# Kernel optimization log

Measured on AMD Instinct MI355X. Metric: run time of the kernel, lower is better.

## Reference

```python
import jax, jax.numpy as jnp
import numpy as np

NH = 16
D = 1024
DKH = D // NH  # 64


def _split_heads(x, nh):
    B, L, d = x.shape
    return x.reshape(B, L, nh, d // nh).transpose(0, 2, 1, 3)  # [B,Nh,L,dh]


def setup_inputs() -> dict:
    key = jax.random.key(0)
    ks = jax.random.split(key, 10)
    B, L, d = 2, 2048, D
    s = 1.0 / np.sqrt(d)
    inp = {
        "q": jax.random.normal(ks[0], (B, L, d), jnp.float32),
        "k": jax.random.normal(ks[1], (B, L, d), jnp.float32),
        "q_mask": jnp.ones((B, L), jnp.float32),
        "k_mask": jnp.ones((B, L), jnp.float32),
        "pos_logits": jax.random.normal(ks[2], (B, L, L), jnp.float32),
        # Linear params (torch convention: y = x @ W.T + b)
        "Wq": jax.random.normal(ks[3], (d, d), jnp.float32) * s,
        "bq": jnp.zeros((d,), jnp.float32),
        "Wk": jax.random.normal(ks[4], (d, d), jnp.float32) * s,
        "bk": jnp.zeros((d,), jnp.float32),
        "Wv": jax.random.normal(ks[5], (d, d), jnp.float32) * s,
        "bv": jnp.zeros((d,), jnp.float32),
        "Wo": jax.random.normal(ks[6], (d, d), jnp.float32) * s,
        "bo": jnp.zeros((d,), jnp.float32),
    }
    return inp


def reference(q, k, q_mask, k_mask, pos_logits, Wq, bq, Wk, bk, Wv, bv, Wo, bo):
    # Projections (note: v is computed from the *projected* k, as in the source)
    qp = (q @ Wq.T + bq) * (DKH ** -0.5)   # [B,Lq,dk]
    kp = k @ Wk.T + bk                     # [B,Lk,dk]
    vp = kp @ Wv.T + bv                    # [B,Lk,dv]

    qh = _split_heads(qp, NH)              # [B,Nh,Lq,dkh]
    kh = _split_heads(kp, NH)              # [B,Nh,Lk,dkh]
    vh = _split_heads(vp, NH)              # [B,Nh,Lk,dvh]

    # Additive attention mask: -inf where q_mask[i]*k_mask[j] == 0
    mask_prod = q_mask[:, :, None] * k_mask[:, None, :]          # [B,Lq,Lk]
    attn_mask = jnp.where(mask_prod == 0, jnp.float32(-jnp.inf), jnp.float32(0.0))[:, None]  # [B,1,Lq,Lk]

    con_logits = jnp.einsum("bhid,bhjd->bhij", qh, kh)           # [B,Nh,Lq,Lk]
    logits = attn_mask + con_logits + pos_logits[:, None]
    weights = jax.nn.softmax(logits, axis=-1)
    attn = jnp.einsum("bhij,bhjd->bhid", weights, vh)            # [B,Nh,Lq,dvh]

    B, Nh, Lq, dvh = attn.shape
    attn = attn.transpose(0, 2, 1, 3).reshape(B, Lq, Nh * dvh)   # combine heads
    out = attn @ Wo.T + bo                                       # output projection
    # dropout is identity in eval mode
    return out
```

## Files before the change

### kernel.cpp

```cpp
#include <hip/hip_runtime.h>
#include <math.h>

#define BB 2
#define LL 2048
#define DMODEL 1024
#define NHEAD 16
#define MTOK 4096
#define KVB 32
#define NT (LL / KVB)

typedef unsigned short u16;
typedef __attribute__((ext_vector_type(8))) short short8;
typedef __attribute__((ext_vector_type(4))) float f32x4;

__device__ __host__ inline u16 f2bf(float f) {
    unsigned u = __builtin_bit_cast(unsigned, f);
    return (u16)((u + 0x7FFFu + ((u >> 16) & 1u)) >> 16);
}
__device__ inline float bf2f(u16 h) {
    unsigned u = ((unsigned)h) << 16;
    return __builtin_bit_cast(float, u);
}

__device__ inline void split_one(const float* __restrict__ x, u16* __restrict__ hi,
                                 u16* __restrict__ lo, int n4)
{
    for (int i = blockIdx.x * blockDim.x + threadIdx.x; i < n4;
         i += gridDim.x * blockDim.x) {
        float4 v = ((const float4*)x)[i];
        ushort4 h, l;
        h.x = f2bf(v.x); l.x = f2bf(v.x - bf2f(h.x));
        h.y = f2bf(v.y); l.y = f2bf(v.y - bf2f(h.y));
        h.z = f2bf(v.z); l.z = f2bf(v.z - bf2f(h.z));
        h.w = f2bf(v.w); l.w = f2bf(v.w - bf2f(h.w));
        ((ushort4*)hi)[i] = h;
        ((ushort4*)lo)[i] = l;
    }
}

__global__ __launch_bounds__(256)
void split_planes2(const float* __restrict__ x0, u16* __restrict__ h0, u16* __restrict__ l0,
                   const float* __restrict__ x1, u16* __restrict__ h1, u16* __restrict__ l1,
                   int n4)
{
    if (blockIdx.y == 0) split_one(x0, h0, l0, n4);
    else                 split_one(x1, h1, l1, n4);
}

__global__ __launch_bounds__(256)
void split_planes4(const float* __restrict__ x0, u16* __restrict__ h0, u16* __restrict__ l0,
                   const float* __restrict__ x1, u16* __restrict__ h1, u16* __restrict__ l1,
                   const float* __restrict__ x2, u16* __restrict__ h2, u16* __restrict__ l2,
                   const float* __restrict__ x3, u16* __restrict__ h3, u16* __restrict__ l3,
                   int n4)
{
    switch (blockIdx.y & 3) {
        case 0: split_one(x0, h0, l0, n4); break;
        case 1: split_one(x1, h1, l1, n4); break;
        case 2: split_one(x2, h2, l2, n4); break;
        default: split_one(x3, h3, l3, n4); break;
    }
}

#define GBM 128
#define GBN 64
#define GBK 32

__global__ __launch_bounds__(256)
void gemm_mfma_split(const u16* __restrict__ Ahi, const u16* __restrict__ Alo,
                     const u16* __restrict__ Bhi, const u16* __restrict__ Blo,
                     const float* __restrict__ bias, float scale, int K, int N,
                     float* __restrict__ Yf, u16* __restrict__ Yhi,
                     u16* __restrict__ Ylo, int mode)
{
    __shared__ u16 lds[2][12288];

    const int tid = threadIdx.x;
    const int lid = tid & 63;
    const int w   = tid >> 6;
    const int wm  = w >> 1, wn = w & 1;
    const int m0  = blockIdx.y * GBM;
    const int n0  = blockIdx.x * GBN;

    f32x4 acc[4][2];
    #pragma unroll
    for (int ms = 0; ms < 4; ++ms)
        #pragma unroll
        for (int ns = 0; ns < 2; ++ns)
            acc[ms][ns] = (f32x4){0.f, 0.f, 0.f, 0.f};

    auto stage = [&](int buf, int t) {
        const int k0 = t * GBK;
        #pragma unroll
        for (int j = 0; j < 6; ++j) {
            const int q = w * 6 + j;
            const u16* plane; int ldsoff, c, R0;
            if (q < 8)       { plane = Ahi; ldsoff = 0;     c = q;      R0 = m0; }
            else if (q < 16) { plane = Alo; ldsoff = 4096;  c = q - 8;  R0 = m0; }
            else if (q < 20) { plane = Bhi; ldsoff = 8192;  c = q - 16; R0 = n0; }
            else             { plane = Blo; ldsoff = 10240; c = q - 20; R0 = n0; }
            const int r  = c * 16 + (lid >> 2);
            const int ci = lid & 3;
            const int kl = ci ^ ((r >> 1) & 3);
            const u16* g = plane + (size_t)(R0 + r) * K + k0 + kl * 8;
            __builtin_amdgcn_global_load_lds(
                (const __attribute__((address_space(1))) void*)g,
                (__attribute__((address_space(3))) void*)(&lds[buf][ldsoff + c * 512]),
                16, 0, 0);
        }
    };

    auto compute = [&](int buf) {
        const u16* L = lds[buf];
        short8 ah[4], al[4], bh[2], bl[2];
        #pragma unroll
        for (int ms = 0; ms < 4; ++ms) {
            const int r   = wm * 64 + ms * 16 + (lid & 15);
            const int off = r * 32 + (((lid >> 4) ^ ((r >> 1) & 3)) * 8);
            ah[ms] = *(const short8*)&L[off];
            al[ms] = *(const short8*)&L[4096 + off];
        }
        #pragma unroll
        for (int ns = 0; ns < 2; ++ns) {
            const int r   = wn * 32 + ns * 16 + (lid & 15);
            const int off = r * 32 + (((lid >> 4) ^ ((r >> 1) & 3)) * 8);
            bh[ns] = *(const short8*)&L[8192 + off];
            bl[ns] = *(const short8*)&L[10240 + off];
        }
        #pragma unroll
        for (int ms = 0; ms < 4; ++ms)
            #pragma unroll
            for (int ns = 0; ns < 2; ++ns) {
                acc[ms][ns] = __builtin_amdgcn_mfma_f32_16x16x32_bf16(al[ms], bh[ns], acc[ms][ns], 0, 0, 0);
                acc[ms][ns] = __builtin_amdgcn_mfma_f32_16x16x32_bf16(ah[ms], bl[ns], acc[ms][ns], 0, 0, 0);
                acc[ms][ns] = __builtin_amdgcn_mfma_f32_16x16x32_bf16(ah[ms], bh[ns], acc[ms][ns], 0, 0, 0);
            }
    };

    const int nt = K / GBK;
    stage(0, 0);
    __syncthreads();
    for (int t = 0; t < nt; ++t) {
        const int buf = t & 1;
        if (t + 1 < nt) stage(buf ^ 1, t + 1);
        compute(buf);
        __syncthreads();
    }

    const int orow = (lid >> 4) * 4;
    #pragma unroll
    for (int ms = 0; ms < 4; ++ms)
        #pragma unroll
        for (int ns = 0; ns < 2; ++ns) {
            const int col = n0 + wn * 32 + ns * 16 + (lid & 15);
            const float bcol = bias[col];
            if (mode == 2) {
                const int r0 = m0 + wm * 64 + ms * 16 + orow;
                unsigned ph[2] = {0, 0}, pl[2] = {0, 0};
                #pragma unroll
                for (int i = 0; i < 4; ++i) {
                    const float y = (acc[ms][ns][i] + bcol) * scale;
                    const u16 hh = f2bf(y);
                    const u16 ll = f2bf(y - bf2f(hh));
                    ph[i >> 1] |= ((unsigned)hh) << ((i & 1) * 16);
                    pl[i >> 1] |= ((unsigned)ll) << ((i & 1) * 16);
                }
                const size_t idx = (size_t)col * MTOK + r0;
                *(uint2*)(Yhi + idx) = make_uint2(ph[0], ph[1]);
                *(uint2*)(Ylo + idx) = make_uint2(pl[0], pl[1]);
            } else {
                #pragma unroll
                for (int i = 0; i < 4; ++i) {
                    const int row = m0 + wm * 64 + ms * 16 + orow + i;
                    const float y = (acc[ms][ns][i] + bcol) * scale;
                    if (mode == 0) {
                        Yf[(size_t)row * N + col] = y;
                    } else {
                        const size_t idx = (size_t)row * N + col;
                        const u16 hh = f2bf(y);
                        Yhi[idx] = hh;
                        Ylo[idx] = f2bf(y - bf2f(hh));
                    }
                }
            }
        }
}

__global__ __launch_bounds__(256, 4)
void attn_mfma3(const u16* __restrict__ qph, const u16* __restrict__ qpl,
                const u16* __restrict__ kph, const u16* __restrict__ kpl,
                const u16* __restrict__ vth, const u16* __restrict__ vtl,
                const float* __restrict__ qmask, const float* __restrict__ kmask,
                const float* __restrict__ pos,
                u16* __restrict__ ach, u16* __restrict__ acl)
{
    __shared__ float pp[4][512];
    __shared__ u16  kvb[2][4][2048];

    const int tid = threadIdx.x;
    const int lid = tid & 63;
    const int w   = tid >> 6;
    const int q16 = lid & 15;
    const int hi4 = lid >> 4;
    const int qt = blockIdx.x, h = blockIdx.y, b = blockIdx.z;
    const int qw = qt * 64 + w * 16;

    short8 qh[2], ql[2];
    #pragma unroll
    for (int ks = 0; ks < 2; ++ks) {
        const size_t off = (size_t)(b * LL + qw + q16) * DMODEL
                         + h * 64 + ks * 32 + hi4 * 8;
        qh[ks] = *(const short8*)(qph + off);
        ql[ks] = *(const short8*)(qpl + off);
    }

    auto stage = [&](int buf, int t) {
        const int k0 = t * KVB;
        u16* dst = &kvb[buf][w][0];
        #pragma unroll
        for (int c = 0; c < 4; ++c) {
            const u16* src;
            if (w < 2) {
                const int r  = c * 8 + (lid >> 3);
                const int sl = (lid & 7) ^ (r & 7);
                src = (w == 0 ? kph : kpl) +
                      (size_t)(b * LL + k0 + r) * DMODEL + h * 64 + sl * 8;
            } else {
                const int r  = c * 16 + (lid >> 2);
                const int sl = (lid & 3) ^ ((r >> 1) & 3);
                src = (w == 2 ? vth : vtl) +
                      (size_t)(h * 64 + r) * MTOK + b * LL + k0 + sl * 8;
            }
            __builtin_amdgcn_global_load_lds(
                (const __attribute__((address_space(1))) void*)src,
                (__attribute__((address_space(3))) void*)(dst + c * 512), 16, 0, 0);
        }
    };

    float m_run = -INFINITY, l_run = 0.f;
    const float qml = qmask[b * LL + qw + q16];

    f32x4 o_acc[4];
    #pragma unroll
    for (int nfd = 0; nfd < 4; ++nfd)
        o_acc[nfd] = (f32x4){0.f, 0.f, 0.f, 0.f};

    stage(0, 0);
    __syncthreads();

    for (int t = 0; t < NT; ++t) {
        const int buf = t & 1;
        const int k0  = t * KVB;

        float4 kmv[2], posr[2];
        #pragma unroll
        for (int nf = 0; nf < 2; ++nf) {
            kmv[nf]  = *(const float4*)(kmask + b * LL + k0 + nf * 16 + hi4 * 4);
            posr[nf] = *(const float4*)(pos +
                ((size_t)(b * LL + qw + q16)) * LL + k0 + nf * 16 + hi4 * 4);
        }

        if (t + 1 < NT) stage(buf ^ 1, t + 1);

        f32x4 s_acc[2];
        s_acc[0] = (f32x4){0.f, 0.f, 0.f, 0.f};
        s_acc[1] = (f32x4){0.f, 0.f, 0.f, 0.f};

        #pragma unroll
        for (int ks = 0; ks < 2; ++ks)
            #pragma unroll
            for (int nf = 0; nf < 2; ++nf) {
                const int r  = nf * 16 + q16;
                const int sl = (ks * 4 + hi4) ^ (r & 7);
                short8 kbh = *(const short8*)(&kvb[buf][0][r * 64 + sl * 8]);
                short8 kbl = *(const short8*)(&kvb[buf][1][r * 64 + sl * 8]);
                s_acc[nf] = __builtin_amdgcn_mfma_f32_16x16x32_bf16(kbl, qh[ks], s_acc[nf], 0, 0, 0);
                s_acc[nf] = __builtin_amdgcn_mfma_f32_16x16x32_bf16(kbh, ql[ks], s_acc[nf], 0, 0, 0);
                s_acc[nf] = __builtin_amdgcn_mfma_f32_16x16x32_bf16(kbh, qh[ks], s_acc[nf], 0, 0, 0);
            }

        {
            float v[2][4];
            #pragma unroll
            for (int nf = 0; nf < 2; ++nf) {
                const float* km = (const float*)&kmv[nf];
                const float* pr = (const float*)&posr[nf];
                #pragma unroll
                for (int i = 0; i < 4; ++i)
                    v[nf][i] = (qml * km[i] == 0.f)
                               ? -INFINITY : s_acc[nf][i] + pr[i];
            }
            float rm = fmaxf(fmaxf(fmaxf(v[0][0], v[0][1]), fmaxf(v[0][2], v[0][3])),
                             fmaxf(fmaxf(v[1][0], v[1][1]), fmaxf(v[1][2], v[1][3])));
            rm = fmaxf(rm, __shfl_xor(rm, 16));
            rm = fmaxf(rm, __shfl_xor(rm, 32));
            const float mn = fmaxf(m_run, rm);
            const float c  = __expf(m_run - mn);
            float ls = 0.f;
            float p[2][4];
            #pragma unroll
            for (int nf = 0; nf < 2; ++nf)
                #pragma unroll
                for (int i = 0; i < 4; ++i) {
                    p[nf][i] = __expf(v[nf][i] - mn);
                    ls += p[nf][i];
                }
            ls += __shfl_xor(ls, 16);
            ls += __shfl_xor(ls, 32);
            l_run = l_run * c + ls;
            m_run = mn;
            #pragma unroll
            for (int nfd = 0; nfd < 4; ++nfd)
                o_acc[nfd] *= c;
            const int r = q16;
            #pragma unroll
            for (int nf = 0; nf < 2; ++nf) {
                const int sl = (nf * 4 + hi4) ^ (r & 7);
                *(f32x4*)&pp[w][r * 32 + sl * 4] =
                    (f32x4){p[nf][0], p[nf][1], p[nf][2], p[nf][3]};
            }
        }

        short8 pah, pal;
        {
            const int r  = q16;
            const int s0 = (hi4 * 2)     ^ (r & 7);
            const int s1 = (hi4 * 2 + 1) ^ (r & 7);
            f32x4 pa = *(const f32x4*)&pp[w][r * 32 + s0 * 4];
            f32x4 pb = *(const f32x4*)&pp[w][r * 32 + s1 * 4];
            float f[8] = {pa[0], pa[1], pa[2], pa[3], pb[0], pb[1], pb[2], pb[3]};
            #pragma unroll
            for (int jj = 0; jj < 8; ++jj) {
                const unsigned u = __builtin_bit_cast(unsigned, f[jj]);
                pah[jj] = (short)(u >> 16);
                const float lof = f[jj] - __builtin_bit_cast(float, u & 0xFFFF0000u);
                pal[jj] = (short)(__builtin_bit_cast(unsigned, lof) >> 16);
            }
        }
        #pragma unroll
        for (int nfd = 0; nfd < 4; ++nfd) {
            const int r  = nfd * 16 + q16;
            const int sl = hi4 ^ ((r >> 1) & 3);
            short8 vbh = *(const short8*)(&kvb[buf][2][r * 32 + sl * 8]);
            short8 vbl = *(const short8*)(&kvb[buf][3][r * 32 + sl * 8]);
            o_acc[nfd] = __builtin_amdgcn_mfma_f32_16x16x32_bf16(vbl, pah, o_acc[nfd], 0, 0, 0);
            o_acc[nfd] = __builtin_amdgcn_mfma_f32_16x16x32_bf16(vbh, pal, o_acc[nfd], 0, 0, 0);
            o_acc[nfd] = __builtin_amdgcn_mfma_f32_16x16x32_bf16(vbh, pah, o_acc[nfd], 0, 0, 0);
        }

        __syncthreads();
    }

    {
        const float inv = 1.0f / l_run;
        const size_t rb = (size_t)(b * LL + qw + q16) * DMODEL + h * 64;
        #pragma unroll
        for (int nfd = 0; nfd < 4; ++nfd) {
            ushort4 hv, lv;
            #pragma unroll
            for (int i = 0; i < 4; ++i) {
                const float y  = o_acc[nfd][i] * inv;
                const u16 hh   = f2bf(y);
                (&hv.x)[i] = hh;
                (&lv.x)[i] = f2bf(y - bf2f(hh));
            }
            *(ushort4*)(ach + rb + nfd * 16 + hi4 * 4) = hv;
            *(ushort4*)(acl + rb + nfd * 16 + hi4 * 4) = lv;
        }
    }
}

extern "C" void kernel_launch(void* const* d_in, const int* in_sizes, int n_in,
                              void* d_out, int out_size, void* d_ws, size_t ws_size,
                              hipStream_t stream)
{
    const float* q     = (const float*)d_in[0];
    const float* k     = (const float*)d_in[1];
    const float* qmask = (const float*)d_in[2];
    const float* kmask = (const float*)d_in[3];
    const float* pos   = (const float*)d_in[4];
    const float* Wq    = (const float*)d_in[5];
    const float* bq    = (const float*)d_in[6];
    const float* Wk    = (const float*)d_in[7];
    const float* bk    = (const float*)d_in[8];
    const float* Wv    = (const float*)d_in[9];
    const float* bv    = (const float*)d_in[10];
    const float* Wo    = (const float*)d_in[11];
    const float* bo    = (const float*)d_in[12];
    float* out = (float*)d_out;

    const size_t P  = (size_t)MTOK * DMODEL;
    const size_t PW = (size_t)DMODEL * DMODEL;

    u16* base = (u16*)d_ws;
    u16* qp_h = base;            u16* qp_l = qp_h + P;
    u16* kp_h = base + 2 * P;    u16* kp_l = kp_h + P;
    u16* bufA = base + 4 * P;
    u16* bufB = base + 6 * P;
    u16* wq_h = base + 8 * P;    u16* wq_l = wq_h + PW;
    u16* wk_h = wq_l + PW;       u16* wk_l = wk_h + PW;
    u16* wv_h = wk_l + PW;       u16* wv_l = wv_h + PW;
    u16* wo_h = wv_l + PW;       u16* wo_l = wo_h + PW;

    split_planes2<<<dim3(1024, 2), 256, 0, stream>>>(
        q, bufA, bufA + P, k, bufB, bufB + P, (int)(P / 4));
    split_planes4<<<dim3(512, 4), 256, 0, stream>>>(
        Wq, wq_h, wq_l, Wk, wk_h, wk_l, Wv, wv_h, wv_l, Wo, wo_h, wo_l,
        (int)(PW / 4));

    const dim3 gb(DMODEL / GBN, MTOK / GBM);
    const dim3 ga(LL / 64, NHEAD, BB);

    gemm_mfma_split<<<gb, 256, 0, stream>>>(bufA, bufA + P, wq_h, wq_l, bq, 0.125f,
                                            DMODEL, DMODEL, nullptr, qp_h, qp_l, 1);
    gemm_mfma_split<<<gb, 256, 0, stream>>>(bufB, bufB + P, wk_h, wk_l, bk, 1.0f,
                                            DMODEL, DMODEL, nullptr, kp_h, kp_l, 1);
    gemm_mfma_split<<<gb, 256, 0, stream>>>(kp_h, kp_l, wv_h, wv_l, bv, 1.0f,
                                            DMODEL, DMODEL, nullptr, bufA, bufA + P, 2);
    attn_mfma3<<<ga, 256, 0, stream>>>(qp_h, qp_l, kp_h, kp_l, bufA, bufA + P,
                                       qmask, kmask, pos, bufB, bufB + P);
    gemm_mfma_split<<<gb, 256, 0, stream>>>(bufB, bufB + P, wo_h, wo_l, bo, 1.0f,
                                            DMODEL, DMODEL, out, nullptr, nullptr, 0);
}
```

Measured before the change: 470.1 us.

## Enlarge GEMM tiles, batch Q/K projections, and double attention KV block

GEMM tiles grow from 128x64 to 128x128 and the Q and K projections run in one launch that picks its operand set from the block index, cutting per-tile reload cost and launch count. The attention kernel doubles the KV block to 64 keys per iteration, which halves the number of barrier and softmax rescale steps, and wraps the MFMA sections in s_setprio. In exchange, LDS use and register pressure rise, occupancy hints drop to 2 blocks per CU, and the GEMM grids shrink, which risks lower occupancy and fewer blocks to fill the GPU.

```diff
diff --git a/kernel.cpp b/kernel.cpp
--- a/kernel.cpp
+++ b/kernel.cpp
@@ -6,7 +6,7 @@
 #define DMODEL 1024
 #define NHEAD 16
 #define MTOK 4096
-#define KVB 32
+#define KVB 64
 #define NT (LL / KVB)
 
 typedef unsigned short u16;
@@ -62,43 +62,56 @@
     }
 }
 
-#define GBM 128
-#define GBN 64
 #define GBK 32
 
-__global__ __launch_bounds__(256)
-void gemm_mfma_split(const u16* __restrict__ Ahi, const u16* __restrict__ Alo,
-                     const u16* __restrict__ Bhi, const u16* __restrict__ Blo,
-                     const float* __restrict__ bias, float scale, int K, int N,
-                     float* __restrict__ Yf, u16* __restrict__ Yhi,
-                     u16* __restrict__ Ylo, int mode)
-{
-    __shared__ u16 lds[2][12288];
+__global__ __launch_bounds__(256, 2)
+void gemm_mfma2(const u16* __restrict__ A0hi, const u16* __restrict__ A0lo,
+                const u16* __restrict__ B0hi, const u16* __restrict__ B0lo,
+                const float* __restrict__ bias0, float scale0,
+                u16* __restrict__ Y0hi, u16* __restrict__ Y0lo,
+                const u16* __restrict__ A1hi, const u16* __restrict__ A1lo,
+                const u16* __restrict__ B1hi, const u16* __restrict__ B1lo,
+                const float* __restrict__ bias1, float scale1,
+                u16* __restrict__ Y1hi, u16* __restrict__ Y1lo,
+                float* __restrict__ Yf, int K, int Nout, int NX0, int mode)
+{
+    __shared__ u16 lds[2][16384];
 
     const int tid = threadIdx.x;
     const int lid = tid & 63;
     const int w   = tid >> 6;
     const int wm  = w >> 1, wn = w & 1;
-    const int m0  = blockIdx.y * GBM;
-    const int n0  = blockIdx.x * GBN;
-
-    f32x4 acc[4][2];
+    const int bx  = blockIdx.x;
+    const int set = (bx >= NX0) ? 1 : 0;
+    const int n0  = (set ? bx - NX0 : bx) * 128;
+    const int m0  = blockIdx.y * 128;
+
+    const u16* Ahi = set ? A1hi : A0hi;
+    const u16* Alo = set ? A1lo : A0lo;
+    const u16* Bhi = set ? B1hi : B0hi;
+    const u16* Blo = set ? B1lo : B0lo;
+    const float* bias = set ? bias1 : bias0;
+    const float scale = set ? scale1 : scale0;
+    u16* Yhi = set ? Y1hi : Y0hi;
+    u16* Ylo = set ? Y1lo : Y0lo;
+
+    f32x4 acc[4][4];
     #pragma unroll
     for (int ms = 0; ms < 4; ++ms)
         #pragma unroll
-        for (int ns = 0; ns < 2; ++ns)
+        for (int ns = 0; ns < 4; ++ns)
             acc[ms][ns] = (f32x4){0.f, 0.f, 0.f, 0.f};
 
     auto stage = [&](int buf, int t) {
         const int k0 = t * GBK;
         #pragma unroll
-        for (int j = 0; j < 6; ++j) {
-            const int q = w * 6 + j;
+        for (int j = 0; j < 8; ++j) {
+            const int q = w * 8 + j;
             const u16* plane; int ldsoff, c, R0;
             if (q < 8)       { plane = Ahi; ldsoff = 0;     c = q;      R0 = m0; }
             else if (q < 16) { plane = Alo; ldsoff = 4096;  c = q - 8;  R0 = m0; }
-            else if (q < 20) { plane = Bhi; ldsoff = 8192;  c = q - 16; R0 = n0; }
-            else             { plane = Blo; ldsoff = 10240; c = q - 20; R0 = n0; }
+            else if (q < 24) { plane = Bhi; ldsoff = 8192;  c = q - 16; R0 = n0; }
+            else             { plane = Blo; ldsoff = 12288; c = q - 24; R0 = n0; }
             const int r  = c * 16 + (lid >> 2);
             const int ci = lid & 3;
             const int kl = ci ^ ((r >> 1) & 3);
@@ -112,7 +125,7 @@
 
     auto compute = [&](int buf) {
         const u16* L = lds[buf];
-        short8 ah[4], al[4], bh[2], bl[2];
+        short8 ah[4], al[4], bh[4], bl[4];
         #pragma unroll
         for (int ms = 0; ms < 4; ++ms) {
             const int r   = wm * 64 + ms * 16 + (lid & 15);
@@ -121,16 +134,16 @@
             al[ms] = *(const short8*)&L[4096 + off];
         }
         #pragma unroll
-        for (int ns = 0; ns < 2; ++ns) {
-            const int r   = wn * 32 + ns * 16 + (lid & 15);
+        for (int ns = 0; ns < 4; ++ns) {
+            const int r   = wn * 64 + ns * 16 + (lid & 15);
             const int off = r * 32 + (((lid >> 4) ^ ((r >> 1) & 3)) * 8);
             bh[ns] = *(const short8*)&L[8192 + off];
-            bl[ns] = *(const short8*)&L[10240 + off];
+            bl[ns] = *(const short8*)&L[12288 + off];
         }
         #pragma unroll
         for (int ms = 0; ms < 4; ++ms)
             #pragma unroll
-            for (int ns = 0; ns < 2; ++ns) {
+            for (int ns = 0; ns < 4; ++ns) {
                 acc[ms][ns] = __builtin_amdgcn_mfma_f32_16x16x32_bf16(al[ms], bh[ns], acc[ms][ns], 0, 0, 0);
                 acc[ms][ns] = __builtin_amdgcn_mfma_f32_16x16x32_bf16(ah[ms], bl[ns], acc[ms][ns], 0, 0, 0);
                 acc[ms][ns] = __builtin_amdgcn_mfma_f32_16x16x32_bf16(ah[ms], bh[ns], acc[ms][ns], 0, 0, 0);
@@ -151,8 +164,8 @@
     #pragma unroll
     for (int ms = 0; ms < 4; ++ms)
         #pragma unroll
-        for (int ns = 0; ns < 2; ++ns) {
-            const int col = n0 + wn * 32 + ns * 16 + (lid & 15);
+        for (int ns = 0; ns < 4; ++ns) {
+            const int col = n0 + wn * 64 + ns * 16 + (lid & 15);
             const float bcol = bias[col];
             if (mode == 2) {
                 const int r0 = m0 + wm * 64 + ms * 16 + orow;
@@ -174,9 +187,9 @@
                     const int row = m0 + wm * 64 + ms * 16 + orow + i;
                     const float y = (acc[ms][ns][i] + bcol) * scale;
                     if (mode == 0) {
-                        Yf[(size_t)row * N + col] = y;
+                        Yf[(size_t)row * Nout + col] = y;
                     } else {
-                        const size_t idx = (size_t)row * N + col;
+                        const size_t idx = (size_t)row * Nout + col;
                         const u16 hh = f2bf(y);
                         Yhi[idx] = hh;
                         Ylo[idx] = f2bf(y - bf2f(hh));
@@ -186,16 +199,16 @@
         }
 }
 
-__global__ __launch_bounds__(256, 4)
-void attn_mfma3(const u16* __restrict__ qph, const u16* __restrict__ qpl,
+__global__ __launch_bounds__(256, 2)
+void attn_mfma4(const u16* __restrict__ qph, const u16* __restrict__ qpl,
                 const u16* __restrict__ kph, const u16* __restrict__ kpl,
                 const u16* __restrict__ vth, const u16* __restrict__ vtl,
                 const float* __restrict__ qmask, const float* __restrict__ kmask,
                 const float* __restrict__ pos,
                 u16* __restrict__ ach, u16* __restrict__ acl)
 {
-    __shared__ float pp[4][512];
-    __shared__ u16  kvb[2][4][2048];
+    __shared__ float pp[4][1024];
+    __shared__ u16  kvb[2][4][4096];
 
     const int tid = threadIdx.x;
     const int lid = tid & 63;
@@ -218,19 +231,14 @@
         const int k0 = t * KVB;
         u16* dst = &kvb[buf][w][0];
         #pragma unroll
-        for (int c = 0; c < 4; ++c) {
+        for (int c = 0; c < 8; ++c) {
+            const int r  = c * 8 + (lid >> 3);
+            const int sp = (lid & 7) ^ (r & 7);
             const u16* src;
-            if (w < 2) {
-                const int r  = c * 8 + (lid >> 3);
-                const int sl = (lid & 7) ^ (r & 7);
-                src = (w == 0 ? kph : kpl) +
-                      (size_t)(b * LL + k0 + r) * DMODEL + h * 64 + sl * 8;
-            } else {
-                const int r  = c * 16 + (lid >> 2);
-                const int sl = (lid & 3) ^ ((r >> 1) & 3);
-                src = (w == 2 ? vth : vtl) +
-                      (size_t)(h * 64 + r) * MTOK + b * LL + k0 + sl * 8;
-            }
+            if (w == 0)      src = kph + (size_t)(b * LL + k0 + r) * DMODEL + h * 64 + sp * 8;
+            else if (w == 1) src = kpl + (size_t)(b * LL + k0 + r) * DMODEL + h * 64 + sp * 8;
+            else if (w == 2) src = vth + (size_t)(h * 64 + r) * MTOK + b * LL + k0 + sp * 8;
+            else             src = vtl + (size_t)(h * 64 + r) * MTOK + b * LL + k0 + sp * 8;
             __builtin_amdgcn_global_load_lds(
                 (const __attribute__((address_space(1))) void*)src,
                 (__attribute__((address_space(3))) void*)(dst + c * 512), 16, 0, 0);
@@ -239,6 +247,8 @@
 
     float m_run = -INFINITY, l_run = 0.f;
     const float qml = qmask[b * LL + qw + q16];
+    const float* prow = pos + (size_t)(b * LL + qw + q16) * LL;
+    const float* kmrow = kmask + b * LL;
 
     f32x4 o_acc[4];
     #pragma unroll
@@ -252,37 +262,40 @@
         const int buf = t & 1;
         const int k0  = t * KVB;
 
-        float4 kmv[2], posr[2];
-        #pragma unroll
-        for (int nf = 0; nf < 2; ++nf) {
-            kmv[nf]  = *(const float4*)(kmask + b * LL + k0 + nf * 16 + hi4 * 4);
-            posr[nf] = *(const float4*)(pos +
-                ((size_t)(b * LL + qw + q16)) * LL + k0 + nf * 16 + hi4 * 4);
+        float4 kmv[4], posr[4];
+        #pragma unroll
+        for (int nf = 0; nf < 4; ++nf) {
+            kmv[nf]  = *(const float4*)(kmrow + k0 + nf * 16 + hi4 * 4);
+            posr[nf] = *(const float4*)(prow + k0 + nf * 16 + hi4 * 4);
         }
 
         if (t + 1 < NT) stage(buf ^ 1, t + 1);
 
-        f32x4 s_acc[2];
-        s_acc[0] = (f32x4){0.f, 0.f, 0.f, 0.f};
-        s_acc[1] = (f32x4){0.f, 0.f, 0.f, 0.f};
-
+        f32x4 s_acc[4];
+        #pragma unroll
+        for (int nf = 0; nf < 4; ++nf)
+            s_acc[nf] = (f32x4){0.f, 0.f, 0.f, 0.f};
+
+        __builtin_amdgcn_s_setprio(1);
         #pragma unroll
         for (int ks = 0; ks < 2; ++ks)
             #pragma unroll
-            for (int nf = 0; nf < 2; ++nf) {
-                const int r  = nf * 16 + q16;
-                const int sl = (ks * 4 + hi4) ^ (r & 7);
-                short8 kbh = *(const short8*)(&kvb[buf][0][r * 64 + sl * 8]);
-                short8 kbl = *(const short8*)(&kvb[buf][1][r * 64 + sl * 8]);
+            for (int nf = 0; nf < 4; ++nf) {
+                const int r   = nf * 16 + q16;
+                const int off = r * 64 + (((ks * 4 + hi4) ^ (r & 7)) * 8);
+                short8 kbh = *(const short8*)(&kvb[buf][0][off]);
+                short8 kbl = *(const short8*)(&kvb[buf][1][off]);
                 s_acc[nf] = __builtin_amdgcn_mfma_f32_16x16x32_bf16(kbl, qh[ks], s_acc[nf], 0, 0, 0);
                 s_acc[nf] = __builtin_amdgcn_mfma_f32_16x16x32_bf16(kbh, ql[ks], s_acc[nf], 0, 0, 0);
                 s_acc[nf] = __builtin_amdgcn_mfma_f32_16x16x32_bf16(kbh, qh[ks], s_acc[nf], 0, 0, 0);
             }
-
+        __builtin_amdgcn_s_setprio(0);
+
+        float p[4][4];
         {
-            float v[2][4];
-            #pragma unroll
-            for (int nf = 0; nf < 2; ++nf) {
+            float v[4][4];
+            #pragma unroll
+            for (int nf = 0; nf < 4; ++nf) {
                 const float* km = (const float*)&kmv[nf];
                 const float* pr = (const float*)&posr[nf];
                 #pragma unroll
@@ -290,16 +303,18 @@
                     v[nf][i] = (qml * km[i] == 0.f)
                                ? -INFINITY : s_acc[nf][i] + pr[i];
             }
-            float rm = fmaxf(fmaxf(fmaxf(v[0][0], v[0][1]), fmaxf(v[0][2], v[0][3])),
-                             fmaxf(fmaxf(v[1][0], v[1][1]), fmaxf(v[1][2], v[1][3])));
+            float rm = -INFINITY;
+            #pragma unroll
+            for (int nf = 0; nf < 4; ++nf)
+                #pragma unroll
+                for (int i = 0; i < 4; ++i) rm = fmaxf(rm, v[nf][i]);
             rm = fmaxf(rm, __shfl_xor(rm, 16));
             rm = fmaxf(rm, __shfl_xor(rm, 32));
             const float mn = fmaxf(m_run, rm);
             const float c  = __expf(m_run - mn);
             float ls = 0.f;
-            float p[2][4];
-            #pragma unroll
-            for (int nf = 0; nf < 2; ++nf)
+            #pragma unroll
+            for (int nf = 0; nf < 4; ++nf)
                 #pragma unroll
                 for (int i = 0; i < 4; ++i) {
                     p[nf][i] = __expf(v[nf][i] - mn);
@@ -312,41 +327,48 @@
             #pragma unroll
             for (int nfd = 0; nfd < 4; ++nfd)
                 o_acc[nfd] *= c;
-            const int r = q16;
-            #pragma unroll
-            for (int nf = 0; nf < 2; ++nf) {
-                const int sl = (nf * 4 + hi4) ^ (r & 7);
-                *(f32x4*)&pp[w][r * 32 + sl * 4] =
-                    (f32x4){p[nf][0], p[nf][1], p[nf][2], p[nf][3]};
-            }
-        }
-
-        short8 pah, pal;
-        {
-            const int r  = q16;
-            const int s0 = (hi4 * 2)     ^ (r & 7);
-            const int s1 = (hi4 * 2 + 1) ^ (r & 7);
-            f32x4 pa = *(const f32x4*)&pp[w][r * 32 + s0 * 4];
-            f32x4 pb = *(const f32x4*)&pp[w][r * 32 + s1 * 4];
+        }
+
+        #pragma unroll
+        for (int nf = 0; nf < 4; ++nf) {
+            const int c4 = (nf * 4 + hi4) ^ q16;
+            *(f32x4*)&pp[w][q16 * 64 + c4 * 4] =
+                (f32x4){p[nf][0], p[nf][1], p[nf][2], p[nf][3]};
+        }
+
+        short8 pah[2], pal[2];
+        #pragma unroll
+        for (int pks = 0; pks < 2; ++pks) {
+            const int c4a = (pks * 8 + hi4 * 2)     ^ q16;
+            const int c4b = (pks * 8 + hi4 * 2 + 1) ^ q16;
+            f32x4 pa = *(const f32x4*)&pp[w][q16 * 64 + c4a * 4];
+            f32x4 pb = *(const f32x4*)&pp[w][q16 * 64 + c4b * 4];
             float f[8] = {pa[0], pa[1], pa[2], pa[3], pb[0], pb[1], pb[2], pb[3]};
+            short8 hv, lv;
             #pragma unroll
             for (int jj = 0; jj < 8; ++jj) {
                 const unsigned u = __builtin_bit_cast(unsigned, f[jj]);
-                pah[jj] = (short)(u >> 16);
+                hv[jj] = (short)(u >> 16);
                 const float lof = f[jj] - __builtin_bit_cast(float, u & 0xFFFF0000u);
-                pal[jj] = (short)(__builtin_bit_cast(unsigned, lof) >> 16);
-            }
-        }
-        #pragma unroll
-        for (int nfd = 0; nfd < 4; ++nfd) {
-            const int r  = nfd * 16 + q16;
-            const int sl = hi4 ^ ((r >> 1) & 3);
-            short8 vbh = *(const short8*)(&kvb[buf][2][r * 32 + sl * 8]);
-            short8 vbl = *(const short8*)(&kvb[buf][3][r * 32 + sl * 8]);
-            o_acc[nfd] = __builtin_amdgcn_mfma_f32_16x16x32_bf16(vbl, pah, o_acc[nfd], 0, 0, 0);
-            o_acc[nfd] = __builtin_amdgcn_mfma_f32_16x16x32_bf16(vbh, pal, o_acc[nfd], 0, 0, 0);
-            o_acc[nfd] = __builtin_amdgcn_mfma_f32_16x16x32_bf16(vbh, pah, o_acc[nfd], 0, 0, 0);
-        }
+                lv[jj] = (short)(__builtin_bit_cast(unsigned, lof) >> 16);
+            }
+            pah[pks] = hv; pal[pks] = lv;
+        }
+
+        __builtin_amdgcn_s_setprio(1);
+        #pragma unroll
+        for (int pks = 0; pks < 2; ++pks)
+            #pragma unroll
+            for (int nfd = 0; nfd < 4; ++nfd) {
+                const int r   = nfd * 16 + q16;
+                const int off = r * 64 + (((pks * 4 + hi4) ^ (r & 7)) * 8);
+                short8 vbh = *(const short8*)(&kvb[buf][2][off]);
+                short8 vbl = *(const short8*)(&kvb[buf][3][off]);
+                o_acc[nfd] = __builtin_amdgcn_mfma_f32_16x16x32_bf16(vbl, pah[pks], o_acc[nfd], 0, 0, 0);
+                o_acc[nfd] = __builtin_amdgcn_mfma_f32_16x16x32_bf16(vbh, pal[pks], o_acc[nfd], 0, 0, 0);
+                o_acc[nfd] = __builtin_amdgcn_mfma_f32_16x16x32_bf16(vbh, pah[pks], o_acc[nfd], 0, 0, 0);
+            }
+        __builtin_amdgcn_s_setprio(0);
 
         __syncthreads();
     }
@@ -408,17 +430,22 @@
         Wq, wq_h, wq_l, Wk, wk_h, wk_l, Wv, wv_h, wv_l, Wo, wo_h, wo_l,
         (int)(PW / 4));
 
-    const dim3 gb(DMODEL / GBN, MTOK / GBM);
+    const dim3 gQK(16, MTOK / 128);
+    const dim3 g1(8,  MTOK / 128);
     const dim3 ga(LL / 64, NHEAD, BB);
 
-    gemm_mfma_split<<<gb, 256, 0, stream>>>(bufA, bufA + P, wq_h, wq_l, bq, 0.125f,
-                                            DMODEL, DMODEL, nullptr, qp_h, qp_l, 1);
-    gemm_mfma_split<<<gb, 256, 0, stream>>>(bufB, bufB + P, wk_h, wk_l, bk, 1.0f,
-                                            DMODEL, DMODEL, nullptr, kp_h, kp_l, 1);
-    gemm_mfma_split<<<gb, 256, 0, stream>>>(kp_h, kp_l, wv_h, wv_l, bv, 1.0f,
-                                            DMODEL, DMODEL, nullptr, bufA, bufA + P, 2);
-    attn_mfma3<<<ga, 256, 0, stream>>>(qp_h, qp_l, kp_h, kp_l, bufA, bufA + P,
+    gemm_mfma2<<<gQK, 256, 0, stream>>>(
+        bufA, bufA + P, wq_h, wq_l, bq, 0.125f, qp_h, qp_l,
+        bufB, bufB + P, wk_h, wk_l, bk, 1.0f,   kp_h, kp_l,
+        nullptr, DMODEL, DMODEL, 8, 1);
+    gemm_mfma2<<<g1, 256, 0, stream>>>(
+        kp_h, kp_l, wv_h, wv_l, bv, 1.0f, bufA, bufA + P,
+        kp_h, kp_l, wv_h, wv_l, bv, 1.0f, bufA, bufA + P,
+        nullptr, DMODEL, DMODEL, 8, 2);
+    attn_mfma4<<<ga, 256, 0, stream>>>(qp_h, qp_l, kp_h, kp_l, bufA, bufA + P,
                                        qmask, kmask, pos, bufB, bufB + P);
-    gemm_mfma_split<<<gb, 256, 0, stream>>>(bufB, bufB + P, wo_h, wo_l, bo, 1.0f,
-                                            DMODEL, DMODEL, out, nullptr, nullptr, 0);
-}
+    gemm_mfma2<<<g1, 256, 0, stream>>>(
+        bufB, bufB + P, wo_h, wo_l, bo, 1.0f, nullptr, nullptr,
+        bufB, bufB + P, wo_h, wo_l, bo, 1.0f, nullptr, nullptr,
+        out, DMODEL, DMODEL, 8, 0);
+}
```

Result: slower. 484.9 us (+3.2%).
